# Kernel tuning notes

Measured on AMD Instinct MI355X. Metric: run time of the kernel, lower is better.

## Reference

```python
import jax, jax.numpy as jnp
import numpy as np

# Static config (matches init_kwargs)
H, G, D = 16, 4, 128          # n_head, n_query_groups, head_size
QPK = H // G                  # queries per kv group = 4
LEFT = 1024 - 1               # sliding-window left width (local_window-1)
SCALE = 1.0 / float(np.sqrt(D))
NEG = jnp.finfo(jnp.float32).min


def _rope(x, cos, sin):
    # x: [B,T,h,D]; cos/sin: [T, D/2]; non-interleaved (flash-attn) convention
    d2 = cos.shape[-1]
    x1, x2 = x[..., :d2], x[..., d2:]
    c = cos[None, :, None, :]
    s = sin[None, :, None, :]
    return jnp.concatenate([x1 * c - x2 * s, x1 * s + x2 * c], axis=-1)


def setup_inputs() -> dict:
    key = jax.random.key(0)
    ks = jax.random.split(key, 4)
    B, T, C = 1, 2048, 2048
    x = jax.random.normal(ks[0], (B, T, C), jnp.float32)
    # real RoPE tables, base 10000
    pos = jnp.arange(T, dtype=jnp.float32)
    inv_freq = 1.0 / (10000.0 ** (jnp.arange(0, D, 2, dtype=jnp.float32) / D))
    ang = pos[:, None] * inv_freq[None, :]        # [T, D/2]
    cos, sin = jnp.cos(ang), jnp.sin(ang)
    W_attn = jax.random.normal(ks[1], ((H + 2 * G) * D, C), jnp.float32) * 0.02
    W_proj = jax.random.normal(ks[2], (C, H * D), jnp.float32) * 0.02
    k_sink = jax.random.normal(ks[3], (G * D,), jnp.float32) * 0.02
    v_sink = jnp.zeros((G * D,), jnp.float32)     # buffer, zeros in original
    return {"x": x, "cos": cos, "sin": sin, "W_attn": W_attn,
            "W_proj": W_proj, "k_sink": k_sink, "v_sink": v_sink}


def reference(x, cos, sin, W_attn, W_proj, k_sink, v_sink):
    B, T, C = x.shape
    # fused QKV projection (no bias)
    qkv = jnp.einsum('btc,oc->bto', x, W_attn)                 # [B,T,(H+2G)*D]
    qkv = qkv.reshape(B, T, G, QPK + 2, D)
    q = qkv[:, :, :, :QPK, :].reshape(B, T, H, D)              # [B,T,H,D]
    k = qkv[:, :, :, QPK, :]                                   # [B,T,G,D]
    v = qkv[:, :, :, QPK + 1, :]                               # [B,T,G,D]
    # RoPE on q and k
    q = _rope(q, cos, sin)
    k = _rope(k, cos, sin)
    # prepend sink token to k/v -> seqlen_k = T+1
    k = jnp.concatenate([jnp.broadcast_to(k_sink.reshape(1, 1, G, D), (B, 1, G, D)), k], axis=1)
    v = jnp.concatenate([jnp.broadcast_to(v_sink.reshape(1, 1, G, D), (B, 1, G, D)), v], axis=1)
    Tk = T + 1
    # GQA: group-major query head layout -> head h uses kv group h // QPK
    kh = jnp.repeat(k, QPK, axis=2)                            # [B,Tk,H,D]
    vh = jnp.repeat(v, QPK, axis=2)
    scores = jnp.einsum('bqhd,bkhd->bhqk', q, kh) * SCALE      # [B,H,T,Tk]
    # flash-attn causal + sliding window, bottom-right aligned: offset = Tk - T
    off = Tk - T
    i = jnp.arange(T)[:, None]
    j = jnp.arange(Tk)[None, :]
    allowed = (j <= i + off) & (j >= i + off - LEFT)
    scores = jnp.where(allowed[None, None], scores, NEG)
    p = jax.nn.softmax(scores, axis=-1)
    o = jnp.einsum('bhqk,bkhd->bqhd', p, vh).reshape(B, T, H * D)
    y = jnp.einsum('btd,cd->btc', o, W_proj)                   # output proj, no bias
    return y
```

## Files before the change

kernel.cpp:

```cpp
#include <hip/hip_runtime.h>

#define T_SEQ  2048
#define JP     2080
#define SL_F    0.12751744f
#define THR_L2  11.0f

typedef __attribute__((ext_vector_type(8))) short short8;
typedef __attribute__((ext_vector_type(4))) float f32x4;
typedef __attribute__((ext_vector_type(4))) int   i32x4;

__device__ __forceinline__ unsigned short f2bf(float f) {
  unsigned int u = __float_as_uint(f);
  u += 0x7fff + ((u >> 16) & 1);
  return (unsigned short)(u >> 16);
}

__device__ __forceinline__ void gload16(const void* g, void* l) {
  __builtin_amdgcn_global_load_lds(
      (const __attribute__((address_space(1))) void*)g,
      (__attribute__((address_space(3))) void*)l, 16, 0, 0);
}

__global__ __launch_bounds__(256) void quant_rows(
    const float* __restrict__ s0, signed char* __restrict__ d0,
    float* __restrict__ sc0, int n0, int p0,
    const float* __restrict__ s1, signed char* __restrict__ d1,
    float* __restrict__ sc1, int n1, int p1) {
  __shared__ float red[4];
  int r = blockIdx.x;
  const float* s; signed char* d; float* sc; int p;
  if (r < n0) { s = s0; d = d0; sc = sc0; p = p0; }
  else { r -= n0; if (r >= n1) return; s = s1; d = d1; sc = sc1; p = p1; }
  const int tid = threadIdx.x;
  const float4* sp = (const float4*)(s + (size_t)r * 2048) + tid * 2;
  float4 v0 = sp[0], v1 = sp[1];
  float vv[8] = {v0.x, v0.y, v0.z, v0.w, v1.x, v1.y, v1.z, v1.w};
  float am = 0.f;
#pragma unroll
  for (int e = 0; e < 8; ++e) am = fmaxf(am, fabsf(vv[e]));
#pragma unroll
  for (int o = 1; o <= 32; o <<= 1) am = fmaxf(am, __shfl_xor(am, o, 64));
  if ((tid & 63) == 0) red[tid >> 6] = am;
  __syncthreads();
  am = fmaxf(fmaxf(red[0], red[1]), fmaxf(red[2], red[3]));
  const float inv = (am > 1e-30f) ? 32512.f / am : 0.f;
  if (tid == 0) sc[r] = am * (1.f / 32512.f);
  int hb[8], lb[8];
#pragma unroll
  for (int e = 0; e < 8; ++e) {
    int n  = __float2int_rn(vv[e] * inv);
    int nh = (n + 128) >> 8;
    hb[e] = nh & 0xff;
    lb[e] = (n - (nh << 8)) & 0xff;
  }
  int2 hw, lw;
  hw.x = hb[0] | (hb[1] << 8) | (hb[2] << 16) | (hb[3] << 24);
  hw.y = hb[4] | (hb[5] << 8) | (hb[6] << 16) | (hb[7] << 24);
  lw.x = lb[0] | (lb[1] << 8) | (lb[2] << 16) | (lb[3] << 24);
  lw.y = lb[4] | (lb[5] << 8) | (lb[6] << 16) | (lb[7] << 24);
  *(int2*)(d + (size_t)r * 2048 + tid * 8)     = hw;
  *(int2*)(d + p + (size_t)r * 2048 + tid * 8) = lw;
}

__global__ __launch_bounds__(256, 2) void gemm_i8(const signed char* __restrict__ Ag,
                                                  const signed char* __restrict__ Bg,
                                                  const float* __restrict__ sav,
                                                  const float* __restrict__ sbv,
                                                  float* __restrict__ C,
                                                  int M, int N, int K) {
  __shared__ signed char Anh[2][128 * 64], Anl[2][128 * 64];
  __shared__ signed char Bnh[2][128 * 64], Bnl[2][128 * 64];

  const int tid  = threadIdx.x;
  const int lane = tid & 63;
  const int wid  = tid >> 6;
  const int wm   = (wid >> 1) << 6;
  const int wn   = (wid & 1) << 6;
  const int lo16 = lane & 15;
  const int hi4  = lane >> 4;
  const int m0   = blockIdx.y << 7;
  const int n0   = blockIdx.x << 7;
  const size_t MK = (size_t)M * K;
  const size_t NK = (size_t)N * K;

  const int r0 = (wid << 4) + (lane >> 2);
  const int r1 = r0 + 64;
  const int cB = (lane & 3) << 4;
  const signed char* a0g = Ag + (size_t)(m0 + r0) * K + cB;
  const signed char* a1g = Ag + (size_t)(m0 + r1) * K + cB;
  const signed char* b0g = Bg + (size_t)(n0 + r0) * K + cB;
  const signed char* b1g = Bg + (size_t)(n0 + r1) * K + cB;
  const int o0 = wid << 10;
  const int o1 = (4 + wid) << 10;

  int ra[4], rb[4];
#pragma unroll
  for (int i = 0; i < 4; ++i) {
    ra[i] = ((wm + i * 16 + lo16) << 6) + (hi4 << 4);
    rb[i] = ((wn + i * 16 + lo16) << 6) + (hi4 << 4);
  }

  i32x4 acc1[4][4], acc2[4][4];
  const i32x4 zi = {0, 0, 0, 0};
#pragma unroll
  for (int i = 0; i < 4; ++i)
#pragma unroll
    for (int j = 0; j < 4; ++j) { acc1[i][j] = zi; acc2[i][j] = zi; }

  gload16(a0g,      &Anh[0][o0]);
  gload16(a1g,      &Anh[0][o1]);
  gload16(a0g + MK, &Anl[0][o0]);
  gload16(a1g + MK, &Anl[0][o1]);
  gload16(b0g,      &Bnh[0][o0]);
  gload16(b1g,      &Bnh[0][o1]);
  gload16(b0g + NK, &Bnl[0][o0]);
  gload16(b1g + NK, &Bnl[0][o1]);

  int cur = 0;
  for (int k0 = 0; k0 < K; k0 += 64) {
    const bool more = (k0 + 64) < K;
    if (more) {
      const int nxt = cur ^ 1;
      const int kn  = k0 + 64;
      gload16(a0g + kn,      &Anh[nxt][o0]);
      gload16(a1g + kn,      &Anh[nxt][o1]);
      gload16(a0g + MK + kn, &Anl[nxt][o0]);
      gload16(a1g + MK + kn, &Anl[nxt][o1]);
      gload16(b0g + kn,      &Bnh[nxt][o0]);
      gload16(b1g + kn,      &Bnh[nxt][o1]);
      gload16(b0g + NK + kn, &Bnl[nxt][o0]);
      gload16(b1g + NK + kn, &Bnl[nxt][o1]);
      asm volatile("s_waitcnt vmcnt(8)" ::: "memory");
    } else {
      asm volatile("s_waitcnt vmcnt(0)" ::: "memory");
    }
    __builtin_amdgcn_s_barrier();
    __builtin_amdgcn_sched_barrier(0);

    i32x4 fah[4], fal[4], fbh[4], fbl[4];
#pragma unroll
    for (int i = 0; i < 4; ++i) {
      fah[i] = *(const i32x4*)&Anh[cur][ra[i]];
      fal[i] = *(const i32x4*)&Anl[cur][ra[i]];
      fbh[i] = *(const i32x4*)&Bnh[cur][rb[i]];
      fbl[i] = *(const i32x4*)&Bnl[cur][rb[i]];
    }
#pragma unroll
    for (int i = 0; i < 4; ++i)
#pragma unroll
      for (int j = 0; j < 4; ++j) {
        acc1[i][j] = __builtin_amdgcn_mfma_i32_16x16x64_i8(fah[i], fbh[j], acc1[i][j], 0, 0, 0);
        acc2[i][j] = __builtin_amdgcn_mfma_i32_16x16x64_i8(fah[i], fbl[j], acc2[i][j], 0, 0, 0);
        acc2[i][j] = __builtin_amdgcn_mfma_i32_16x16x64_i8(fal[i], fbh[j], acc2[i][j], 0, 0, 0);
      }

    __builtin_amdgcn_sched_barrier(0);
    __builtin_amdgcn_s_barrier();
    asm volatile("" ::: "memory");
    cur ^= 1;
  }

#pragma unroll
  for (int i = 0; i < 4; ++i) {
    const int rowb = m0 + wm + i * 16 + (hi4 << 2);
    float sa0 = sav[rowb], sa1 = sav[rowb + 1], sa2 = sav[rowb + 2], sa3 = sav[rowb + 3];
#pragma unroll
    for (int j = 0; j < 4; ++j) {
      const int col = n0 + wn + j * 16 + lo16;
      const float sb = sbv[col];
      float* cp = C + (size_t)rowb * N + col;
      cp[0]           = fmaf(65536.f, (float)acc1[i][j][0], 256.f * (float)acc2[i][j][0]) * sa0 * sb;
      cp[(size_t)N]   = fmaf(65536.f, (float)acc1[i][j][1], 256.f * (float)acc2[i][j][1]) * sa1 * sb;
      cp[(size_t)2*N] = fmaf(65536.f, (float)acc1[i][j][2], 256.f * (float)acc2[i][j][2]) * sa2 * sb;
      cp[(size_t)3*N] = fmaf(65536.f, (float)acc1[i][j][3], 256.f * (float)acc2[i][j][3]) * sa3 * sb;
    }
  }
}

#define RB_Q  4096
#define RB_K  1024
#define RB_KE 64
#define RB_V  65

__global__ __launch_bounds__(256) void rope2(const float* __restrict__ qkv,
                                             const float* __restrict__ cosb,
                                             const float* __restrict__ sinb,
                                             const float* __restrict__ ksink,
                                             const float* __restrict__ vsink,
                                             unsigned short* __restrict__ qb,
                                             unsigned short* __restrict__ kb,
                                             unsigned short* __restrict__ vtb) {
  __shared__ unsigned short tl[512 * 33];
  const int bid = blockIdx.x, tid = threadIdx.x;
  if (bid < RB_Q) {
    int idx = bid * 256 + tid;
    int t = idx >> 9, rem = idx & 511;
    int h = rem >> 5, dp = (rem & 31) << 1;
    int g = h >> 2, qi = h & 3;
    const float* src = qkv + (size_t)t * 3072 + g * 768 + qi * 128;
    float2 x1 = *(const float2*)(src + dp);
    float2 x2 = *(const float2*)(src + 64 + dp);
    float2 c  = *(const float2*)(cosb + t * 64 + dp);
    float2 s  = *(const float2*)(sinb + t * 64 + dp);
    ushort2 o1 = { f2bf(x1.x * c.x - x2.x * s.x), f2bf(x1.y * c.y - x2.y * s.y) };
    ushort2 o2 = { f2bf(x1.x * s.x + x2.x * c.x), f2bf(x1.y * s.y + x2.y * c.y) };
    *(ushort2*)(qb + (size_t)t * 2048 + h * 128 + dp)      = o1;
    *(ushort2*)(qb + (size_t)t * 2048 + h * 128 + 64 + dp) = o2;
  } else if (bid < RB_Q + RB_K) {
    int idx = (bid - RB_Q) * 256 + tid;
    int t = idx >> 7, rem = idx & 127;
    int g = rem >> 5, dp = (rem & 31) << 1;
    const float* src = qkv + (size_t)t * 3072 + g * 768 + 512;
    float2 x1 = *(const float2*)(src + dp);
    float2 x2 = *(const float2*)(src + 64 + dp);
    float2 c  = *(const float2*)(cosb + t * 64 + dp);
    float2 s  = *(const float2*)(sinb + t * 64 + dp);
    ushort2 o1 = { f2bf(x1.x * c.x - x2.x * s.x), f2bf(x1.y * c.y - x2.y * s.y) };
    ushort2 o2 = { f2bf(x1.x * s.x + x2.x * c.x), f2bf(x1.y * s.y + x2.y * c.y) };
    size_t base = (size_t)(t + 1) * 512 + g * 128 + dp;
    *(ushort2*)(kb + base)      = o1;
    *(ushort2*)(kb + base + 64) = o2;
  } else if (bid < RB_Q + RB_K + RB_KE) {
    int idx = (bid - RB_Q - RB_K) * 256 + tid;
    int jj = idx >> 9, c = idx & 511;
    if (jj == 0) kb[c] = f2bf(ksink[c]);
    else         kb[(size_t)(2048 + jj) * 512 + c] = 0;
  } else {
    int b  = bid - RB_Q - RB_K - RB_KE;
    int j0 = b << 5;
#pragma unroll 4
    for (int st = 0; st < 64; ++st) {
      int id = st * 256 + tid;
      int jj = id >> 9, c = id & 511;
      int j = j0 + jj;
      float val;
      if (j == 0)          val = vsink[c];
      else if (j <= T_SEQ) val = qkv[(size_t)(j - 1) * 3072 + (c >> 7) * 768 + 640 + (c & 127)];
      else                 val = 0.f;
      tl[c * 33 + jj] = f2bf(val);
    }
    __syncthreads();
#pragma unroll 4
    for (int st = 0; st < 32; ++st) {
      int id = st * 256 + tid;
      int row = id >> 4, jp = (id & 15) << 1;
      ushort2 w = { tl[row * 33 + jp], tl[row * 33 + jp + 1] };
      *(ushort2*)(vtb + (size_t)row * JP + j0 + jp) = w;
    }
  }
}

#define KSTR 136
#define VSTR 40

__global__ __launch_bounds__(512) void attn_mfma_bf16(const unsigned short* __restrict__ qb,
                                                      const unsigned short* __restrict__ kb,
                                                      const unsigned short* __restrict__ vtb,
                                                      float* __restrict__ of) {
  __shared__ unsigned short Kl[2][32 * KSTR];
  __shared__ unsigned short Vl[2][128 * VSTR];

  const int bid  = blockIdx.x;
  const int tid  = threadIdx.x;
  const int tile = bid >> 2;
  const int g    = bid & 3;
  const int t0b  = tile << 5;
  const int wv   = tid >> 6;
  const int hq   = wv & 3;
  const int sub  = wv >> 2;
  const int h    = g * 4 + hq;
  const int lane = tid & 63;
  const int lo   = lane & 15;
  const int hi   = lane >> 4;
  const int t0w  = t0b + (sub << 4);
  const int t    = t0w + lo;

  const int sj   = tid >> 4;
  const int sc   = (tid & 15) << 3;
  const int kphi = ((((sj & 7) << 2) | (sj >> 3))) * KSTR + sc;
  const int svd  = tid >> 2;
  const int svj  = (tid & 3) << 3;
  const int vdst = svd * VSTR + svj;
  const unsigned short* ksrc = kb  + (size_t)sj * 512 + g * 128 + sc;
  const unsigned short* vsrc = vtb + (size_t)(g * 128 + svd) * JP + svj;

  short8 qfrag[4];
  {
    const unsigned short* qp = qb + (size_t)t * 2048 + h * 128 + (hi << 3);
#pragma unroll
    for (int d0 = 0; d0 < 4; ++d0) qfrag[d0] = *(const short8*)(qp + d0 * 32);
  }

  f32x4 acc[8];
  const f32x4 z4 = {0.f, 0.f, 0.f, 0.f};
#pragma unroll
  for (int dt = 0; dt < 8; ++dt) acc[dt] = z4;

  float m = -1e4f, l = 0.f;

  int jlo = t0b - 1022; if (jlo < 0) jlo = 0;
  const int jb0  = jlo & ~31;
  const int jmax = t0b + 32;
  const int nch  = ((jmax - jb0) >> 5) + 1;

  const int klA = (((lo & 3) << 2) | (lo >> 2)) * KSTR + (hi << 3);

  uint4 kreg = *(const uint4*)(ksrc + (size_t)jb0 * 512);
  uint4 vreg = *(const uint4*)(vsrc + jb0);
  *(uint4*)&Kl[0][kphi] = kreg;
  *(uint4*)&Vl[0][vdst] = vreg;
  __syncthreads();

  int bsel = 0;
  for (int ci = 0; ci < nch; ++ci) {
    const int jb = jb0 + (ci << 5);
    const bool more = (ci + 1 < nch);
    if (more) {
      const int jn = jb + 32;
      kreg = *(const uint4*)(ksrc + (size_t)jn * 512);
      vreg = *(const uint4*)(vsrc + jn);
    }

    const unsigned short* Kb = &Kl[bsel][0];
    f32x4 sa = z4, sb = z4;
#pragma unroll
    for (int d0 = 0; d0 < 4; ++d0) {
      short8 ka  = *(const short8*)(Kb + klA + d0 * 32);
      short8 kB2 = *(const short8*)(Kb + klA + 16 * KSTR + d0 * 32);
      sa = __builtin_amdgcn_mfma_f32_16x16x32_bf16(ka,  qfrag[d0], sa, 0, 0, 0);
      sb = __builtin_amdgcn_mfma_f32_16x16x32_bf16(kB2, qfrag[d0], sb, 0, 0, 0);
    }

    float z[8];
    const int jbase = jb + (hi << 3);
    const bool interior = (jb >= t0w - 1007) && (jb <= t0w - 30);
    if (interior) {
#pragma unroll
      for (int r = 0; r < 4; ++r) { z[r] = sa[r] * SL_F; z[r + 4] = sb[r] * SL_F; }
    } else {
#pragma unroll
      for (int r = 0; r < 8; ++r) {
        float sv = (r < 4) ? sa[r] : sb[r - 4];
        int j = jbase + r;
        bool valid = (j <= t + 1) && (j >= t - 1022);
        z[r] = valid ? sv * SL_F : -1e30f;
      }
    }

    float lmax = fmaxf(fmaxf(fmaxf(z[0], z[1]), fmaxf(z[2], z[3])),
                       fmaxf(fmaxf(z[4], z[5]), fmaxf(z[6], z[7])));
    if (!__all(lmax <= m + THR_L2)) {
      float cm = lmax;
      cm = fmaxf(cm, __shfl_xor(cm, 16, 64));
      cm = fmaxf(cm, __shfl_xor(cm, 32, 64));
      float mn = fmaxf(m, cm);
      float a  = exp2f(m - mn);
      l *= a;
#pragma unroll
      for (int dt = 0; dt < 8; ++dt) acc[dt] *= a;
      m = mn;
    }

    float p[8];
#pragma unroll
    for (int r = 0; r < 8; ++r) { p[r] = exp2f(z[r] - m); l += p[r]; }

    short8 pfrag;
#pragma unroll
    for (int e = 0; e < 8; ++e) pfrag[e] = (short)f2bf(p[e]);

    const unsigned short* Vb = &Vl[bsel][0];
#pragma unroll
    for (int dt = 0; dt < 8; ++dt) {
      short8 vf = *(const short8*)(Vb + (dt * 16 + lo) * VSTR + (hi << 3));
      acc[dt] = __builtin_amdgcn_mfma_f32_16x16x32_bf16(vf, pfrag, acc[dt], 0, 0, 0);
    }

    if (more) {
      *(uint4*)&Kl[bsel ^ 1][kphi] = kreg;
      *(uint4*)&Vl[bsel ^ 1][vdst] = vreg;
      __syncthreads();
      bsel ^= 1;
    }
  }

  float lt = l;
  lt += __shfl_xor(lt, 16, 64);
  lt += __shfl_xor(lt, 32, 64);
  const float inv = 1.f / lt;

  float* op = of + (size_t)t * 2048 + h * 128 + (hi << 2);
#pragma unroll
  for (int dt = 0; dt < 8; ++dt) {
    f32x4 o4 = acc[dt] * inv;
    *(f32x4*)(op + dt * 16) = o4;
  }
}

extern "C" void kernel_launch(void* const* d_in, const int* in_sizes, int n_in,
                              void* d_out, int out_size, void* d_ws, size_t ws_size,
                              hipStream_t stream) {
  const float* x     = (const float*)d_in[0];
  const float* cosb  = (const float*)d_in[1];
  const float* sinb  = (const float*)d_in[2];
  const float* Wa    = (const float*)d_in[3];
  const float* Wp    = (const float*)d_in[4];
  const float* ksink = (const float*)d_in[5];
  const float* vsink = (const float*)d_in[6];
  float* y = (float*)d_out;

  char* ws = (char*)d_ws;
  float*          qkv = (float*)ws;
  float*          of  = (float*)ws;
  signed char*    ops = (signed char*)(ws + 16777216);
  signed char*    was = (signed char*)(ws + 25165824);
  signed char*    wps = (signed char*)(ws + 25165824);
  signed char*    xs  = (signed char*)(ws + 38748736);
  unsigned short* qb  = (unsigned short*)(ws + 38748736);
  unsigned short* kbb = (unsigned short*)(ws + 47137344);
  unsigned short* vtb = (unsigned short*)(ws + 49267264);
  float*          s_x  = (float*)(ws + 51397184);
  float*          s_wa = (float*)(ws + 51405376);
  float*          s_wp = (float*)(ws + 51417664);
  float*          s_o  = (float*)(ws + 51425856);

  quant_rows<<<5120, 256, 0, stream>>>(x, xs, s_x, 2048, 4194304,
                                       Wa, was, s_wa, 3072, 6291456);
  gemm_i8<<<dim3(24, 16), 256, 0, stream>>>(xs, was, s_x, s_wa, qkv, 2048, 3072, 2048);
  rope2<<<RB_Q + RB_K + RB_KE + RB_V, 256, 0, stream>>>(qkv, cosb, sinb, ksink, vsink,
                                                        qb, kbb, vtb);
  quant_rows<<<2048, 256, 0, stream>>>(Wp, wps, s_wp, 2048, 4194304,
                                       Wp, wps, s_wp, 0, 0);
  attn_mfma_bf16<<<256, 512, 0, stream>>>(qb, kbb, vtb, of);
  quant_rows<<<2048, 256, 0, stream>>>(of, ops, s_o, 2048, 4194304,
                                       of, ops, s_o, 0, 0);
  gemm_i8<<<dim3(16, 16), 256, 0, stream>>>(ops, wps, s_o, s_wp, y, 2048, 2048, 2048);
}
```

Baseline: 282.2 us.

## Fuse output quantization into attention, merge quant launches, split-K output GEMM

Attention now writes its output directly as two-plane int8 using a global scale derived from the max |V| (computed in rope2), removing the fp32 output write and separate quant pass. All three quantization passes (x, W_attn, W_proj) are merged into one launch. The output projection GEMM uses split-K over 2 slices with atomicAdd into a zeroed output to double block count. Risks: a per-tensor V-based scale instead of a per-row scale loses precision, and atomics plus a memset add traffic and nondeterminism.

```diff
diff --git a/kernel.cpp b/kernel.cpp
--- a/kernel.cpp
+++ b/kernel.cpp
@@ -21,19 +21,19 @@
       (__attribute__((address_space(3))) void*)l, 16, 0, 0);
 }
 
-__global__ __launch_bounds__(256) void quant_rows(
-    const float* __restrict__ s0, signed char* __restrict__ d0,
-    float* __restrict__ sc0, int n0, int p0,
-    const float* __restrict__ s1, signed char* __restrict__ d1,
-    float* __restrict__ sc1, int n1, int p1) {
+__global__ __launch_bounds__(256) void quant3(
+    const float* __restrict__ sx, signed char* __restrict__ dx, float* __restrict__ scx,
+    const float* __restrict__ sa, signed char* __restrict__ da, float* __restrict__ sca,
+    const float* __restrict__ sp, signed char* __restrict__ dp, float* __restrict__ scp) {
   __shared__ float red[4];
   int r = blockIdx.x;
   const float* s; signed char* d; float* sc; int p;
-  if (r < n0) { s = s0; d = d0; sc = sc0; p = p0; }
-  else { r -= n0; if (r >= n1) return; s = s1; d = d1; sc = sc1; p = p1; }
+  if (r < 2048)      { s = sx; d = dx; sc = scx; p = 4194304; }
+  else if (r < 5120) { r -= 2048; s = sa; d = da; sc = sca; p = 6291456; }
+  else               { r -= 5120; s = sp; d = dp; sc = scp; p = 4194304; }
   const int tid = threadIdx.x;
-  const float4* sp = (const float4*)(s + (size_t)r * 2048) + tid * 2;
-  float4 v0 = sp[0], v1 = sp[1];
+  const float4* spv = (const float4*)(s + (size_t)r * 2048) + tid * 2;
+  float4 v0 = spv[0], v1 = spv[1];
   float vv[8] = {v0.x, v0.y, v0.z, v0.w, v1.x, v1.y, v1.z, v1.w};
   float am = 0.f;
 #pragma unroll
@@ -67,7 +67,8 @@
                                                   const float* __restrict__ sav,
                                                   const float* __restrict__ sbv,
                                                   float* __restrict__ C,
-                                                  int M, int N, int K) {
+                                                  int M, int N, int K,
+                                                  int kLen, int saUniform, int useAtomic) {
   __shared__ signed char Anh[2][128 * 64], Anl[2][128 * 64];
   __shared__ signed char Bnh[2][128 * 64], Bnl[2][128 * 64];
 
@@ -80,16 +81,17 @@
   const int hi4  = lane >> 4;
   const int m0   = blockIdx.y << 7;
   const int n0   = blockIdx.x << 7;
+  const int kOff = blockIdx.z * kLen;
   const size_t MK = (size_t)M * K;
   const size_t NK = (size_t)N * K;
 
   const int r0 = (wid << 4) + (lane >> 2);
   const int r1 = r0 + 64;
   const int cB = (lane & 3) << 4;
-  const signed char* a0g = Ag + (size_t)(m0 + r0) * K + cB;
-  const signed char* a1g = Ag + (size_t)(m0 + r1) * K + cB;
-  const signed char* b0g = Bg + (size_t)(n0 + r0) * K + cB;
-  const signed char* b1g = Bg + (size_t)(n0 + r1) * K + cB;
+  const signed char* a0g = Ag + (size_t)(m0 + r0) * K + cB + kOff;
+  const signed char* a1g = Ag + (size_t)(m0 + r1) * K + cB + kOff;
+  const signed char* b0g = Bg + (size_t)(n0 + r0) * K + cB + kOff;
+  const signed char* b1g = Bg + (size_t)(n0 + r1) * K + cB + kOff;
   const int o0 = wid << 10;
   const int o1 = (4 + wid) << 10;
 
@@ -117,8 +119,8 @@
   gload16(b1g + NK, &Bnl[0][o1]);
 
   int cur = 0;
-  for (int k0 = 0; k0 < K; k0 += 64) {
-    const bool more = (k0 + 64) < K;
+  for (int k0 = 0; k0 < kLen; k0 += 64) {
+    const bool more = (k0 + 64) < kLen;
     if (more) {
       const int nxt = cur ^ 1;
       const int kn  = k0 + 64;
@@ -160,19 +162,33 @@
     cur ^= 1;
   }
 
+  const float saU = saUniform ? sav[0] : 0.f;
 #pragma unroll
   for (int i = 0; i < 4; ++i) {
     const int rowb = m0 + wm + i * 16 + (hi4 << 2);
-    float sa0 = sav[rowb], sa1 = sav[rowb + 1], sa2 = sav[rowb + 2], sa3 = sav[rowb + 3];
+    float sa0, sa1, sa2, sa3;
+    if (saUniform) { sa0 = sa1 = sa2 = sa3 = saU; }
+    else { sa0 = sav[rowb]; sa1 = sav[rowb + 1]; sa2 = sav[rowb + 2]; sa3 = sav[rowb + 3]; }
 #pragma unroll
     for (int j = 0; j < 4; ++j) {
       const int col = n0 + wn + j * 16 + lo16;
       const float sb = sbv[col];
       float* cp = C + (size_t)rowb * N + col;
-      cp[0]           = fmaf(65536.f, (float)acc1[i][j][0], 256.f * (float)acc2[i][j][0]) * sa0 * sb;
-      cp[(size_t)N]   = fmaf(65536.f, (float)acc1[i][j][1], 256.f * (float)acc2[i][j][1]) * sa1 * sb;
-      cp[(size_t)2*N] = fmaf(65536.f, (float)acc1[i][j][2], 256.f * (float)acc2[i][j][2]) * sa2 * sb;
-      cp[(size_t)3*N] = fmaf(65536.f, (float)acc1[i][j][3], 256.f * (float)acc2[i][j][3]) * sa3 * sb;
+      float v0 = fmaf(65536.f, (float)acc1[i][j][0], 256.f * (float)acc2[i][j][0]) * sa0 * sb;
+      float v1 = fmaf(65536.f, (float)acc1[i][j][1], 256.f * (float)acc2[i][j][1]) * sa1 * sb;
+      float v2 = fmaf(65536.f, (float)acc1[i][j][2], 256.f * (float)acc2[i][j][2]) * sa2 * sb;
+      float v3 = fmaf(65536.f, (float)acc1[i][j][3], 256.f * (float)acc2[i][j][3]) * sa3 * sb;
+      if (useAtomic) {
+        atomicAdd(cp, v0);
+        atomicAdd(cp + (size_t)N, v1);
+        atomicAdd(cp + (size_t)2 * N, v2);
+        atomicAdd(cp + (size_t)3 * N, v3);
+      } else {
+        cp[0]           = v0;
+        cp[(size_t)N]   = v1;
+        cp[(size_t)2*N] = v2;
+        cp[(size_t)3*N] = v3;
+      }
     }
   }
 }
@@ -189,8 +205,10 @@
                                              const float* __restrict__ vsink,
                                              unsigned short* __restrict__ qb,
                                              unsigned short* __restrict__ kb,
-                                             unsigned short* __restrict__ vtb) {
+                                             unsigned short* __restrict__ vtb,
+                                             float* __restrict__ vamax) {
   __shared__ unsigned short tl[512 * 33];
+  __shared__ float vred[4];
   const int bid = blockIdx.x, tid = threadIdx.x;
   if (bid < RB_Q) {
     int idx = bid * 256 + tid;
@@ -228,6 +246,7 @@
   } else {
     int b  = bid - RB_Q - RB_K - RB_KE;
     int j0 = b << 5;
+    float am = 0.f;
 #pragma unroll 4
     for (int st = 0; st < 64; ++st) {
       int id = st * 256 + tid;
@@ -237,9 +256,15 @@
       if (j == 0)          val = vsink[c];
       else if (j <= T_SEQ) val = qkv[(size_t)(j - 1) * 3072 + (c >> 7) * 768 + 640 + (c & 127)];
       else                 val = 0.f;
+      am = fmaxf(am, fabsf(val));
       tl[c * 33 + jj] = f2bf(val);
     }
+#pragma unroll
+    for (int o = 1; o <= 32; o <<= 1) am = fmaxf(am, __shfl_xor(am, o, 64));
+    if ((tid & 63) == 0) vred[tid >> 6] = am;
     __syncthreads();
+    if (tid == 0)
+      vamax[b] = fmaxf(fmaxf(vred[0], vred[1]), fmaxf(vred[2], vred[3]));
 #pragma unroll 4
     for (int st = 0; st < 32; ++st) {
       int id = st * 256 + tid;
@@ -256,7 +281,9 @@
 __global__ __launch_bounds__(512) void attn_mfma_bf16(const unsigned short* __restrict__ qb,
                                                       const unsigned short* __restrict__ kb,
                                                       const unsigned short* __restrict__ vtb,
-                                                      float* __restrict__ of) {
+                                                      signed char* __restrict__ ops,
+                                                      const float* __restrict__ vamax,
+                                                      float* __restrict__ s_oq) {
   __shared__ unsigned short Kl[2][32 * KSTR];
   __shared__ unsigned short Vl[2][128 * VSTR];
 
@@ -275,6 +302,14 @@
   const int t0w  = t0b + (sub << 4);
   const int t    = t0w + lo;
 
+  float vam = 0.f;
+  for (int i = lane; i < 65; i += 64) vam = fmaxf(vam, vamax[i]);
+#pragma unroll
+  for (int o = 1; o <= 32; o <<= 1) vam = fmaxf(vam, __shfl_xor(vam, o, 64));
+  const float s_eff = vam * 1.00390625f;
+  const float invq  = (vam > 1e-30f) ? 32512.f / s_eff : 0.f;
+  if (bid == 0 && tid == 0) *s_oq = s_eff * (1.f / 32512.f);
+
   const int sj   = tid >> 4;
   const int sc   = (tid & 15) << 3;
   const int kphi = ((((sj & 7) << 2) | (sj >> 3))) * KSTR + sc;
@@ -389,11 +424,22 @@
   lt += __shfl_xor(lt, 32, 64);
   const float inv = 1.f / lt;
 
-  float* op = of + (size_t)t * 2048 + h * 128 + (hi << 2);
+  const size_t elem = (size_t)t * 2048 + h * 128 + (hi << 2);
 #pragma unroll
   for (int dt = 0; dt < 8; ++dt) {
     f32x4 o4 = acc[dt] * inv;
-    *(f32x4*)(op + dt * 16) = o4;
+    int hb[4], lb[4];
+#pragma unroll
+    for (int e = 0; e < 4; ++e) {
+      int n  = __float2int_rn(o4[e] * invq);
+      int nh = (n + 128) >> 8;
+      hb[e] = nh & 0xff;
+      lb[e] = (n - (nh << 8)) & 0xff;
+    }
+    int hw = hb[0] | (hb[1] << 8) | (hb[2] << 16) | (hb[3] << 24);
+    int lw = lb[0] | (lb[1] << 8) | (lb[2] << 16) | (lb[3] << 24);
+    *(int*)(ops + elem + dt * 16)           = hw;
+    *(int*)(ops + 4194304 + elem + dt * 16) = lw;
   }
 }
 
@@ -411,28 +457,26 @@
 
   char* ws = (char*)d_ws;
   float*          qkv = (float*)ws;
-  float*          of  = (float*)ws;
-  signed char*    ops = (signed char*)(ws + 16777216);
-  signed char*    was = (signed char*)(ws + 25165824);
-  signed char*    wps = (signed char*)(ws + 25165824);
-  signed char*    xs  = (signed char*)(ws + 38748736);
-  unsigned short* qb  = (unsigned short*)(ws + 38748736);
-  unsigned short* kbb = (unsigned short*)(ws + 47137344);
-  unsigned short* vtb = (unsigned short*)(ws + 49267264);
-  float*          s_x  = (float*)(ws + 51397184);
-  float*          s_wa = (float*)(ws + 51405376);
-  float*          s_wp = (float*)(ws + 51417664);
-  float*          s_o  = (float*)(ws + 51425856);
-
-  quant_rows<<<5120, 256, 0, stream>>>(x, xs, s_x, 2048, 4194304,
-                                       Wa, was, s_wa, 3072, 6291456);
-  gemm_i8<<<dim3(24, 16), 256, 0, stream>>>(xs, was, s_x, s_wa, qkv, 2048, 3072, 2048);
+  signed char*    ops = (signed char*)ws;
+  signed char*    xs  = (signed char*)(ws + 25165824);
+  unsigned short* qb  = (unsigned short*)(ws + 25165824);
+  signed char*    was = (signed char*)(ws + 34214432);
+  unsigned short* kbb = (unsigned short*)(ws + 34214432);
+  unsigned short* vtb = (unsigned short*)(ws + 36344352);
+  signed char*    wps = (signed char*)(ws + 46797344);
+  float*          s_x   = (float*)(ws + 55185952);
+  float*          s_wa  = (float*)(ws + 55194144);
+  float*          s_wp  = (float*)(ws + 55206432);
+  float*          vamax = (float*)(ws + 55214624);
+  float*          s_oq  = (float*)(ws + 55215136);
+
+  hipMemsetAsync(y, 0, out_size, stream);
+  quant3<<<7168, 256, 0, stream>>>(x, xs, s_x, Wa, was, s_wa, Wp, wps, s_wp);
+  gemm_i8<<<dim3(24, 16, 1), 256, 0, stream>>>(xs, was, s_x, s_wa, qkv,
+                                               2048, 3072, 2048, 2048, 0, 0);
   rope2<<<RB_Q + RB_K + RB_KE + RB_V, 256, 0, stream>>>(qkv, cosb, sinb, ksink, vsink,
-                                                        qb, kbb, vtb);
-  quant_rows<<<2048, 256, 0, stream>>>(Wp, wps, s_wp, 2048, 4194304,
-                                       Wp, wps, s_wp, 0, 0);
-  attn_mfma_bf16<<<256, 512, 0, stream>>>(qb, kbb, vtb, of);
-  quant_rows<<<2048, 256, 0, stream>>>(of, ops, s_o, 2048, 4194304,
-                                       of, ops, s_o, 0, 0);
-  gemm_i8<<<dim3(16, 16), 256, 0, stream>>>(ops, wps, s_o, s_wp, y, 2048, 2048, 2048);
-}
+                                                        qb, kbb, vtb, vamax);
+  attn_mfma_bf16<<<256, 512, 0, stream>>>(qb, kbb, vtb, ops, vamax, s_oq);
+  gemm_i8<<<dim3(16, 16, 2), 256, 0, stream>>>(ops, wps, s_oq, s_wp, y,
+                                               2048, 2048, 2048, 1024, 1, 1);
+}
```

After: 284.2 us. Within noise of the previous version (+0.7%).
